# Optimization experiments

Measured on AMD Instinct MI355X. Metric: run time of the kernel, lower is better.

Reference implementation:

```python
import jax, jax.numpy as jnp
import numpy as np

BS, T, N, E = 4, 6, 400, 3000
D = 100        # object_dim == state_dim == out_fts (forced by code)
NS = 30        # num states
NOBJ = 300     # object vocab
NET = 10       # n edge types
NSTEPS = 3     # GatedGraphConv n_steps


def setup_inputs() -> dict:
    key = jax.random.key(0)
    ks = jax.random.split(key, 16)
    def nrm(k, shape, s=0.05):
        return jax.random.normal(k, shape, jnp.float32) * s
    return dict(
        class_names=jax.random.randint(ks[0], (BS, T, N), 0, NOBJ),
        states=jax.random.uniform(ks[1], (BS, T, N, NS), jnp.float32),
        edges=jax.random.randint(ks[2], (BS, T, E, 2), 0, N),
        edge_types=jax.random.randint(ks[3], (BS, T, E), 0, NET),
        visibility=jax.random.uniform(ks[4], (BS, T, N), jnp.float32),
        mask_edges=jnp.ones((BS, T, E), jnp.float32),
        obj_emb=nrm(ks[5], (NOBJ, D)),
        state_W=nrm(ks[6], (D, NS)), state_b=jnp.zeros((D,), jnp.float32),
        c1_W=nrm(ks[7], (D, 2 * D)), c1_b=jnp.zeros((D,), jnp.float32),
        c2_W=nrm(ks[8], (D, D)), c2_b=jnp.zeros((D,), jnp.float32),
        edge_embed=nrm(ks[9], (NET, D * D)),
        g_wih=nrm(ks[10], (3 * D, D)), g_whh=nrm(ks[11], (3 * D, D)),
        g_bih=jnp.zeros((3 * D,), jnp.float32), g_bhh=jnp.zeros((3 * D,), jnp.float32),
        o_wih=nrm(ks[12], (3 * D, D)), o_whh=nrm(ks[13], (3 * D, D)),
    )


def _gru(x, h, wih, whh, bih=None, bhh=None):
    # torch.nn.GRUCell semantics
    gi = x @ wih.T
    gh = h @ whh.T
    if bih is not None:
        gi = gi + bih
        gh = gh + bhh
    ir, iz, inn = jnp.split(gi, 3, axis=-1)
    hr, hz, hn = jnp.split(gh, 3, axis=-1)
    r = jax.nn.sigmoid(ir + hr)
    z = jax.nn.sigmoid(iz + hz)
    n = jnp.tanh(inn + r * hn)
    return (1.0 - z) * n + z * h


def reference(class_names, states, edges, edge_types, visibility, mask_edges,
              obj_emb, state_W, state_b, c1_W, c1_b, c2_W, c2_b,
              edge_embed, g_wih, g_whh, g_bih, g_bhh, o_wih, o_whh):
    bs, t_len, n = class_names.shape
    # initial node representation (ClassNameStateRepresentation)
    emb = obj_emb[class_names]                       # [bs,T,N,D]
    st = states @ state_W.T + state_b                # [bs,T,N,D]
    x = jnp.concatenate([emb, st], -1)
    x = jax.nn.relu(x @ c1_W.T + c1_b) @ c2_W.T + c2_b  # [bs,T,N,D]

    off = (jnp.arange(bs) * n)[:, None]              # flatten batch into node axis
    h = jnp.zeros((bs * n, D), x.dtype)              # outer temporal GRU state
    reprs = []
    for t in range(t_len):
        h = _gru(x[:, t].reshape(bs * n, D), h, o_wih, o_whh)  # bias=False
        feat_flat = h                                 # [bs*N, D]
        src = (edges[:, t, :, 0] + off).reshape(-1)   # [bs*E]
        dst = (edges[:, t, :, 1] + off).reshape(-1)
        # per-edge DxD matrices, masked (as in original)
        W = edge_embed[edge_types[:, t].reshape(-1)].reshape(-1, D, D)
        W = W * mask_edges[:, t].reshape(-1)[:, None, None]
        # NOTE: original never updates feat_flat inside the n_steps loop,
        # so every step reads the same source features; we replicate that.
        feat_out = feat_flat
        for _ in range(NSTEPS):
            msg = jnp.einsum('eij,ej->ei', W, feat_flat[src])           # per-edge matvec
            a = jax.ops.segment_sum(msg, dst, num_segments=bs * n)     # scatter-add
            feat_out = _gru(a, feat_flat, g_wih, g_whh, g_bih, g_bhh)
        reprs.append(feat_out.reshape(bs, n, D) * visibility[:, t, :, None])
    node_reprs = jnp.stack(reprs, 1)                  # [bs,T,N,D]
    num_nodes = visibility.sum(-1) + 1e-9             # [bs,T]
    global_repr = (node_reprs * visibility[..., None]).sum(2) / num_nodes[..., None]
    return node_reprs, global_repr
```

## Files before the change

kernel.cpp:

```cpp
#include <hip/hip_runtime.h>

#define BSZ   4
#define TT    6
#define NNODE 400
#define EED   3000
#define DDIM  100
#define NSDIM 30
#define NETYP 10
#define BN    (BSZ*NNODE)
#define NROW  (BSZ*TT*NNODE)
#define NEDGE (BSZ*TT*EED)
#define KPAD  1024

#define OFF_PRE1 0
#define OFF_QT   30000
#define OFF_BQ   33000
#define OFF_BF   33104
#define OFF_WIT  33408
#define OFF_BI   63408
#define OFF_BH   63744
#define OFF_WFH  64080
#define OFF_WFL  85584
#define OFF_WOH  107088
#define OFF_WOL  128592
#define OFF_BWF  150096
#define OFF_BWPK 450096
#define OFF_WHPK 622128
#define OFF_HALL 643632
#define OFF_START 1603632
#define OFF_SE   1613236
#define OFF_INV  1757248
#define OFF_GI   1757280
#define OFF_UB   4982880

typedef __attribute__((ext_vector_type(8))) short bf16x8;
typedef __attribute__((ext_vector_type(4))) float f32x4;

__device__ __forceinline__ float sigf(float v) { return 1.0f / (1.0f + expf(-v)); }

__device__ __forceinline__ short bfc(float f) {
    union { float f; unsigned u; } v; v.f = f;
    unsigned r = v.u + 0x7fffu + ((v.u >> 16) & 1u);
    return (short)(r >> 16);
}

__device__ __forceinline__ float bf2f(short h) {
    union { unsigned u; float f; } x; x.u = ((unsigned)(unsigned short)h) << 16;
    return x.f;
}

__device__ __forceinline__ unsigned cvtpk(float lo, float hi) {
    unsigned r;
    asm("v_cvt_pk_bf16_f32 %0, %1, %2" : "=v"(r) : "v"(lo), "v"(hi));
    return r;
}

__global__ __launch_bounds__(256) void k_front(
    const float* __restrict__ obj_emb, const float* __restrict__ c1_W,
    const float* __restrict__ c1_b, const float* __restrict__ state_W,
    const float* __restrict__ state_b, const float* __restrict__ c2_W,
    const float* __restrict__ c2_b, const float* __restrict__ o_wih,
    const float* __restrict__ o_whh, const float* __restrict__ g_wih,
    const float* __restrict__ g_bih, const float* __restrict__ g_bhh,
    const float* __restrict__ vis, const int* __restrict__ edges,
    const int* __restrict__ etype, const float* __restrict__ emask,
    float* __restrict__ pre1, float* __restrict__ QT, float* __restrict__ bQ,
    float* __restrict__ bfold, float* __restrict__ WiT,
    float* __restrict__ bI, float* __restrict__ bH,
    ushort* __restrict__ WFH, ushort* __restrict__ WFL,
    ushort* __restrict__ WOH, ushort* __restrict__ WOL,
    float* __restrict__ inv_nv, float* __restrict__ gout,
    int* __restrict__ start, int2* __restrict__ sortedE2) {
    int tid = threadIdx.x;
    if (blockIdx.x < 24) {
        __shared__ int hcnt[400];
        __shared__ int hstart[400];
        int c = blockIdx.x;
        int t = c >> 2, b = c & 3;
        int febase = (b * TT + t) * EED;
        for (int i = tid; i < 400; i += 256) hcnt[i] = 0;
        __syncthreads();
        for (int i = tid; i < EED; i += 256)
            atomicAdd(&hcnt[edges[(febase + i) * 2 + 1]], 1);
        __syncthreads();
        if (tid < 64) {
            int lane = tid, carry = 0;
            for (int ch = 0; ch < 7; ++ch) {
                int idx = ch * 64 + lane;
                int orig = (idx < 400) ? hcnt[idx] : 0;
                int v = orig;
                #pragma unroll
                for (int off = 1; off < 64; off <<= 1) {
                    int u = __shfl_up(v, off, 64);
                    if (lane >= off) v += u;
                }
                if (idx < 400) hstart[idx] = carry + (v - orig);
                carry += __shfl(v, 63, 64);
            }
        }
        __syncthreads();
        for (int i = tid; i < 400; i += 256) {
            start[c * 400 + i] = c * EED + hstart[i];
            hcnt[i] = hstart[i];
        }
        if (c == 23 && tid == 0) start[NROW] = NEDGE;
        __syncthreads();
        for (int i = tid; i < EED; i += 256) {
            int fe = febase + i;
            int2 ed = *(const int2*)(edges + fe * 2);
            int pos = atomicAdd(&hcnt[ed.y], 1);
            int g = etype[fe];
            float m = emask[fe];
            sortedE2[c * EED + pos] = make_int2(ed.x | (g << 16), __float_as_int(m));
        }
        return;
    }
    int i = (blockIdx.x - 24) * 256 + tid;
    if (i < 30000) {
        int cls = i / DDIM, d1 = i % DDIM;
        float acc = 0.f;
        for (int k = 0; k < DDIM; ++k)
            acc += obj_emb[cls * DDIM + k] * c1_W[d1 * 2 * DDIM + k];
        pre1[i] = acc;
    } else if (i < 33000) {
        int j = i - 30000, s = j / DDIM, d1 = j % DDIM;
        float acc = 0.f;
        for (int d = 0; d < DDIM; ++d)
            acc += c1_W[d1 * 2 * DDIM + DDIM + d] * state_W[d * NSDIM + s];
        QT[j] = acc;
    } else if (i < 33100) {
        int d1 = i - 33000;
        float acc = c1_b[d1];
        for (int d = 0; d < DDIM; ++d)
            acc += state_b[d] * c1_W[d1 * 2 * DDIM + DDIM + d];
        bQ[d1] = acc;
    } else if (i < 33400) {
        int o = i - 33100;
        float acc = 0.f;
        for (int d = 0; d < DDIM; ++d)
            acc += o_wih[o * DDIM + d] * c2_b[d];
        bfold[o] = acc;
    } else if (i < 76408) {
        int e = i - 33400;
        int j = e & 7, frag = e >> 3;
        int l = frag & 63, ct = (frag >> 6) % 21, kt = frag / (21 * 64);
        int col = ct * 16 + (l & 15);
        int gate = col / 112, dd = col % 112;
        int k = kt * 32 + ((l >> 4) << 3) + j;
        float v = 0.f;
        if (k < DDIM && dd < DDIM) {
            int o = gate * DDIM + dd;
            for (int d = 0; d < DDIM; ++d)
                v += o_wih[o * DDIM + d] * c2_W[d * DDIM + k];
        }
        short hi = bfc(v);
        WFH[frag * 8 + j] = (ushort)hi;
        WFL[frag * 8 + j] = (ushort)bfc(v - bf2f(hi));
    } else if (i < 119416) {
        int e = i - 76408;
        int j = e & 7, frag = e >> 3;
        int l = frag & 63, ct = (frag >> 6) % 21, kt = frag / (21 * 64);
        int col = ct * 16 + (l & 15);
        int gate = col / 112, dd = col % 112;
        int k = kt * 32 + ((l >> 4) << 3) + j;
        float v = 0.f;
        if (k < DDIM && dd < DDIM)
            v = o_whh[(gate * DDIM + dd) * DDIM + k];
        short hi = bfc(v);
        WOH[frag * 8 + j] = (ushort)hi;
        WOL[frag * 8 + j] = (ushort)bfc(v - bf2f(hi));
    } else if (i < 149416) {
        int j = i - 119416, k = j / 300, o = j % 300;
        WiT[j] = g_wih[o * DDIM + k];
    } else if (i < 149752) {
        int col = i - 149416, gate = col / 112, o = col % 112;
        bI[col] = (o < DDIM) ? g_bih[gate * DDIM + o] : 0.f;
    } else if (i < 150088) {
        int col = i - 149752, gate = col / 112, o = col % 112;
        bH[col] = (o < DDIM) ? g_bhh[gate * DDIM + o] : 0.f;
    } else if (i >= 150144 && i < 151680) {
        int g = (i - 150144) >> 6;
        int lane = i & 63;
        float s = 0.f;
        for (int n = lane; n < NNODE; n += 64)
            s += vis[g * NNODE + n];
        #pragma unroll
        for (int off = 32; off > 0; off >>= 1)
            s += __shfl_down(s, off, 64);
        if (lane == 0) inv_nv[g] = 1.f / (s + 1e-9f);
    } else if (i >= 151680 && i < 154080) {
        gout[i - 151680] = 0.f;
    }
}

__global__ __launch_bounds__(448) void k_mid(
    const float* __restrict__ edge_embed, const float* __restrict__ WiT,
    float* __restrict__ BW,
    const int* __restrict__ cls, const float* __restrict__ states,
    const float* __restrict__ pre1, const float* __restrict__ QT,
    const float* __restrict__ bQ, const float* __restrict__ bfold,
    const bf16x8* __restrict__ WFH, const bf16x8* __restrict__ WFL,
    float* __restrict__ GI) {
    __shared__ float st_lds[16 * NSDIM];
    __shared__ float hid_lds[16 * 112];
    __shared__ int cls_lds[16];
    int tid = threadIdx.x;
    if (blockIdx.x < 670) {
        int i = blockIdx.x * 448 + tid;
        if (i < 1000 * 300) {
            int kk = i / 300, go = i % 300;
            int g = kk / DDIM, k = kk % DDIM;
            const float* es = edge_embed + g * DDIM * DDIM + k;
            float acc = 0.f;
            for (int j = 0; j < DDIM; ++j)
                acc += es[j * DDIM] * WiT[j * 300 + go];
            BW[i] = acc;
        }
        return;
    }
    int r0 = (blockIdx.x - 670) * 16;
    for (int idx = tid; idx < 16 * NSDIM; idx += 448) st_lds[idx] = states[r0 * NSDIM + idx];
    if (tid < 16) cls_lds[tid] = cls[r0 + tid];
    __syncthreads();
    #pragma unroll
    for (int u = 0; u < 4; ++u) {
        int it = tid + u * 448;
        if (it < 1600) {
            int n = it / 100, d = it % 100;
            float acc = bQ[d] + pre1[cls_lds[n] * DDIM + d];
            for (int s = 0; s < NSDIM; ++s)
                acc += QT[s * DDIM + d] * st_lds[n * NSDIM + s];
            hid_lds[n * 112 + d] = fmaxf(acc, 0.f);
        }
    }
    __syncthreads();
    int w = tid >> 6, l = tid & 63, rit = l & 15, kgrp = l >> 4;
    f32x4 acc3[3];
    acc3[0] = acc3[1] = acc3[2] = (f32x4){0.f, 0.f, 0.f, 0.f};
    for (int kt = 0; kt < 4; ++kt) {
        bf16x8 Ahi, Alo;
        #pragma unroll
        for (int j = 0; j < 8; ++j) {
            int k = kt * 32 + kgrp * 8 + j;
            float v = (k < DDIM) ? hid_lds[rit * 112 + k] : 0.f;
            short hi = bfc(v);
            Ahi[j] = hi;
            Alo[j] = bfc(v - bf2f(hi));
        }
        #pragma unroll
        for (int p = 0; p < 3; ++p) {
            int ct = w + p * 7;
            bf16x8 Bhi = WFH[(kt * 21 + ct) * 64 + l];
            bf16x8 Blo = WFL[(kt * 21 + ct) * 64 + l];
            acc3[p] = __builtin_amdgcn_mfma_f32_16x16x32_bf16(Ahi, Bhi, acc3[p], 0, 0, 0);
            acc3[p] = __builtin_amdgcn_mfma_f32_16x16x32_bf16(Alo, Bhi, acc3[p], 0, 0, 0);
            acc3[p] = __builtin_amdgcn_mfma_f32_16x16x32_bf16(Ahi, Blo, acc3[p], 0, 0, 0);
        }
    }
    int dd = w * 16 + rit;
    if (dd < DDIM) {
        int b = r0 / (TT * NNODE), t = (r0 / NNODE) % TT, nn0 = r0 % NNODE;
        int trow0 = t * BN + b * NNODE + nn0;
        #pragma unroll
        for (int p = 0; p < 3; ++p) {
            float bias = bfold[p * DDIM + dd];
            #pragma unroll
            for (int j = 0; j < 4; ++j) {
                int row = kgrp * 4 + j;
                GI[(trow0 + row) * 336 + p * 112 + dd] = acc3[p][j] + bias;
            }
        }
    }
}

__global__ __launch_bounds__(448) void k_mid2(const float* __restrict__ GI,
    const bf16x8* __restrict__ WOH, const bf16x8* __restrict__ WOL,
    float* __restrict__ Hall,
    const float* __restrict__ BW, const float* __restrict__ g_whh,
    bf16x8* __restrict__ BWpk, bf16x8* __restrict__ WHpk) {
    __shared__ float h_lds[16 * 112];
    int tid = threadIdx.x;
    if (blockIdx.x >= 100) {
        int i = (blockIdx.x - 100) * 448 + tid;
        if (i < 43008) {
            int l = i & 63, c = (i >> 6) % 21, kt = i / (21 * 64);
            int col = c * 16 + (l & 15);
            int gate = col / 112, o = col % 112;
            bf16x8 r;
            #pragma unroll
            for (int j = 0; j < 8; ++j) {
                int kk = kt * 32 + ((l >> 4) << 3) + j;
                float v = (kk < 1000 && o < DDIM) ? BW[kk * 300 + gate * DDIM + o] : 0.f;
                r[j] = bfc(v);
            }
            BWpk[i] = r;
        } else if (i < 48384) {
            int id = i - 43008;
            int l = id & 63, c = (id >> 6) % 21, kt2 = id / (21 * 64);
            int col = c * 16 + (l & 15);
            int gate = col / 112, o = col % 112;
            bf16x8 r;
            #pragma unroll
            for (int j = 0; j < 8; ++j) {
                int k = kt2 * 32 + ((l >> 4) << 3) + j;
                float v = (k < DDIM && o < DDIM) ? g_whh[(gate * DDIM + o) * DDIM + k] : 0.f;
                r[j] = bfc(v);
            }
            WHpk[id] = r;
        }
        return;
    }
    int bn0 = blockIdx.x * 16;
    for (int idx = tid; idx < 16 * 112; idx += 448) h_lds[idx] = 0.f;
    __syncthreads();
    int w = tid >> 6, l = tid & 63, rit = l & 15, kgrp = l >> 4;
    int dd = w * 16 + rit;
    for (int t = 0; t < TT; ++t) {
        float gir[4], giz[4], gin[4], hold[4];
        if (dd < DDIM) {
            #pragma unroll
            for (int j = 0; j < 4; ++j) {
                int node = kgrp * 4 + j;
                int trow = t * BN + bn0 + node;
                gir[j] = GI[trow * 336 + dd];
                giz[j] = GI[trow * 336 + 112 + dd];
                gin[j] = GI[trow * 336 + 224 + dd];
                hold[j] = h_lds[node * 112 + dd];
            }
        }
        f32x4 a0 = (f32x4){0.f, 0.f, 0.f, 0.f};
        f32x4 a1 = (f32x4){0.f, 0.f, 0.f, 0.f};
        f32x4 a2 = (f32x4){0.f, 0.f, 0.f, 0.f};
        if (t > 0) {
            for (int kt = 0; kt < 4; ++kt) {
                bf16x8 Ahi, Alo;
                #pragma unroll
                for (int j = 0; j < 8; ++j) {
                    int k = kt * 32 + kgrp * 8 + j;
                    float v = (k < DDIM) ? h_lds[rit * 112 + k] : 0.f;
                    short hi = bfc(v);
                    Ahi[j] = hi;
                    Alo[j] = bfc(v - bf2f(hi));
                }
                {
                    bf16x8 Bhi = WOH[(kt * 21 + w) * 64 + l];
                    bf16x8 Blo = WOL[(kt * 21 + w) * 64 + l];
                    a0 = __builtin_amdgcn_mfma_f32_16x16x32_bf16(Ahi, Bhi, a0, 0, 0, 0);
                    a0 = __builtin_amdgcn_mfma_f32_16x16x32_bf16(Alo, Bhi, a0, 0, 0, 0);
                    a0 = __builtin_amdgcn_mfma_f32_16x16x32_bf16(Ahi, Blo, a0, 0, 0, 0);
                }
                {
                    bf16x8 Bhi = WOH[(kt * 21 + w + 7) * 64 + l];
                    bf16x8 Blo = WOL[(kt * 21 + w + 7) * 64 + l];
                    a1 = __builtin_amdgcn_mfma_f32_16x16x32_bf16(Ahi, Bhi, a1, 0, 0, 0);
                    a1 = __builtin_amdgcn_mfma_f32_16x16x32_bf16(Alo, Bhi, a1, 0, 0, 0);
                    a1 = __builtin_amdgcn_mfma_f32_16x16x32_bf16(Ahi, Blo, a1, 0, 0, 0);
                }
                {
                    bf16x8 Bhi = WOH[(kt * 21 + w + 14) * 64 + l];
                    bf16x8 Blo = WOL[(kt * 21 + w + 14) * 64 + l];
                    a2 = __builtin_amdgcn_mfma_f32_16x16x32_bf16(Ahi, Bhi, a2, 0, 0, 0);
                    a2 = __builtin_amdgcn_mfma_f32_16x16x32_bf16(Alo, Bhi, a2, 0, 0, 0);
                    a2 = __builtin_amdgcn_mfma_f32_16x16x32_bf16(Ahi, Blo, a2, 0, 0, 0);
                }
            }
        }
        __syncthreads();
        if (dd < DDIM) {
            #pragma unroll
            for (int j = 0; j < 4; ++j) {
                int node = kgrp * 4 + j;
                int trow = t * BN + bn0 + node;
                float r = sigf(gir[j] + a0[j]);
                float z = sigf(giz[j] + a1[j]);
                float nn = tanhf(gin[j] + r * a2[j]);
                float hnew = (1.f - z) * nn + z * hold[j];
                h_lds[node * 112 + dd] = hnew;
                Hall[trow * DDIM + dd] = hnew;
            }
        }
        __syncthreads();
    }
}

__global__ __launch_bounds__(256) void k_gather(
    const int* __restrict__ start, const int2* __restrict__ sortedE2,
    const float* __restrict__ Hall, unsigned* __restrict__ Ub2) {
    int gid = blockIdx.x * 256 + threadIdx.x;
    int trd = gid >> 6, l = gid & 63;
    int s0 = start[trd], s1 = start[trd + 1];
    int rowbase = (trd / NNODE) * NNODE;
    float acc[16];
    #pragma unroll
    for (int j = 0; j < 16; ++j) acc[j] = 0.f;
    for (int e0 = s0; e0 < s1; e0 += 4) {
        float2 hA[4], hB[4];
        float me[4];
        int ge[4];
        #pragma unroll
        for (int e = 0; e < 4; ++e) {
            int idx = e0 + e;
            int2 rec = (idx < s1) ? sortedE2[idx] : make_int2(0, 0);
            int src = rec.x & 0xffff;
            int g = rec.x >> 16;
            ge[e] = g;
            me[e] = __int_as_float(rec.y);
            const float* hs = Hall + (size_t)(rowbase + src) * DDIM;
            int k0 = g * 100;
            int J0 = k0 >> 7, J1 = (k0 + 99) >> 7;
            int sA = 128 * J0 + 2 * l, sB = 128 * J1 + 2 * l;
            bool aA = (sA >= k0) && (sA < k0 + 100);
            bool aB = (J1 != J0) && (sB >= k0) && (sB < k0 + 100);
            hA[e] = aA ? *(const float2*)(hs + (sA - k0)) : make_float2(0.f, 0.f);
            hB[e] = aB ? *(const float2*)(hs + (sB - k0)) : make_float2(0.f, 0.f);
        }
        #pragma unroll
        for (int e = 0; e < 4; ++e) {
            float m = me[e];
            float ax = m * hA[e].x, ay = m * hA[e].y;
            float bx = m * hB[e].x, by = m * hB[e].y;
            switch (ge[e]) {
                case 0: acc[0] += ax; acc[1] += ay; break;
                case 1: acc[0] += ax; acc[1] += ay; acc[2] += bx; acc[3] += by; break;
                case 2: acc[2] += ax; acc[3] += ay; acc[4] += bx; acc[5] += by; break;
                case 3: acc[4] += ax; acc[5] += ay; acc[6] += bx; acc[7] += by; break;
                case 4: acc[6] += ax; acc[7] += ay; break;
                case 5: acc[6] += ax; acc[7] += ay; acc[8] += bx; acc[9] += by; break;
                case 6: acc[8] += ax; acc[9] += ay; acc[10] += bx; acc[11] += by; break;
                case 7: acc[10] += ax; acc[11] += ay; acc[12] += bx; acc[13] += by; break;
                case 8: acc[12] += ax; acc[13] += ay; acc[14] += bx; acc[15] += by; break;
                case 9: acc[14] += ax; acc[15] += ay; break;
            }
        }
    }
    unsigned* urow = Ub2 + (size_t)trd * 512;
    #pragma unroll
    for (int j = 0; j < 8; ++j)
        urow[64 * j + l] = cvtpk(acc[2 * j], acc[2 * j + 1]);
}

__global__ __launch_bounds__(448) void k_fused32(const ushort* __restrict__ Ub,
    const bf16x8* __restrict__ BWpk, const bf16x8* __restrict__ WHpk,
    const float* __restrict__ bI, const float* __restrict__ bH,
    const float* __restrict__ Hall, const float* __restrict__ visv,
    const float* __restrict__ inv_nv, float* __restrict__ out,
    float* __restrict__ gout) {
    __shared__ unsigned lds[16384];
    int tid = threadIdx.x;
    int w = tid >> 6, l = tid & 63;
    int rit = l & 15, kgrp = l >> 4;
    int rbase = blockIdx.x * 32;

    for (int i = tid; i < 4096; i += 448) {
        int row = i >> 7, g16 = i & 127;
        int4 wv = *(const int4*)(Ub + (size_t)(rbase + row) * KPAD + g16 * 8);
        int wd = row * 512 + ((g16 * 4) ^ ((row & 7) << 2));
        *(int4*)&lds[wd] = wv;
    }
    __syncthreads();

    f32x4 acc[2][3];
    #pragma unroll
    for (int mt = 0; mt < 2; ++mt)
        #pragma unroll
        for (int q = 0; q < 3; ++q) acc[mt][q] = (f32x4){0.f, 0.f, 0.f, 0.f};

    for (int kt = 0; kt < 32; ++kt) {
        bf16x8 fb0 = BWpk[(kt * 21 + w) * 64 + l];
        bf16x8 fb1 = BWpk[(kt * 21 + w + 7) * 64 + l];
        bf16x8 fb2 = BWpk[(kt * 21 + w + 14) * 64 + l];
        #pragma unroll
        for (int mt = 0; mt < 2; ++mt) {
            int row = mt * 16 + rit;
            int wd = row * 512 + (((kt * 16 + kgrp * 4)) ^ ((row & 7) << 2));
            bf16x8 fa = *(bf16x8*)&lds[wd];
            acc[mt][0] = __builtin_amdgcn_mfma_f32_16x16x32_bf16(fa, fb0, acc[mt][0], 0, 0, 0);
            acc[mt][1] = __builtin_amdgcn_mfma_f32_16x16x32_bf16(fa, fb1, acc[mt][1], 0, 0, 0);
            acc[mt][2] = __builtin_amdgcn_mfma_f32_16x16x32_bf16(fa, fb2, acc[mt][2], 0, 0, 0);
        }
    }
    __syncthreads();

    for (int i = tid; i < 512; i += 448) {
        int row = i >> 4, g16 = i & 15;
        int k0 = g16 * 8;
        const float* hs = Hall + (size_t)(rbase + row) * DDIM;
        float v[8];
        #pragma unroll
        for (int jj = 0; jj < 8; ++jj)
            v[jj] = (k0 + jj < DDIM) ? hs[k0 + jj] : 0.f;
        int4 wv;
        wv.x = (int)cvtpk(v[0], v[1]);
        wv.y = (int)cvtpk(v[2], v[3]);
        wv.z = (int)cvtpk(v[4], v[5]);
        wv.w = (int)cvtpk(v[6], v[7]);
        int wd = row * 64 + ((g16 * 4) ^ ((row & 7) << 2));
        *(int4*)&lds[wd] = wv;
    }
    __syncthreads();

    f32x4 hacc[2];
    hacc[0] = (f32x4){0.f, 0.f, 0.f, 0.f};
    hacc[1] = (f32x4){0.f, 0.f, 0.f, 0.f};
    for (int kt2 = 0; kt2 < 4; ++kt2) {
        bf16x8 fb0 = WHpk[(kt2 * 21 + w) * 64 + l];
        bf16x8 fb1 = WHpk[(kt2 * 21 + w + 7) * 64 + l];
        bf16x8 fb2 = WHpk[(kt2 * 21 + w + 14) * 64 + l];
        #pragma unroll
        for (int mt = 0; mt < 2; ++mt) {
            int row = mt * 16 + rit;
            int wd = row * 64 + (((kt2 * 16 + kgrp * 4)) ^ ((row & 7) << 2));
            bf16x8 fh = *(bf16x8*)&lds[wd];
            acc[mt][0] = __builtin_amdgcn_mfma_f32_16x16x32_bf16(fh, fb0, acc[mt][0], 0, 0, 0);
            acc[mt][1] = __builtin_amdgcn_mfma_f32_16x16x32_bf16(fh, fb1, acc[mt][1], 0, 0, 0);
            hacc[mt]  = __builtin_amdgcn_mfma_f32_16x16x32_bf16(fh, fb2, hacc[mt], 0, 0, 0);
        }
    }

    int col = w * 16 + rit;
    if (col < DDIM) {
        float bIr = bI[col], bIz = bI[112 + col], bIn = bI[224 + col];
        float bHr = bH[col], bHz = bH[112 + col], bHn = bH[224 + col];
        int t = rbase / BN;
        #pragma unroll
        for (int mt = 0; mt < 2; ++mt) {
            int r2 = (rbase + mt * 16) % BN;
            int b = r2 / NNODE, n0 = r2 % NNODE;
            int bt = b * TT + t;
            int trow0 = rbase + mt * 16 + kgrp * 4;
            int brow0 = bt * NNODE + n0 + kgrp * 4;
            float gs = 0.f;
            #pragma unroll
            for (int j = 0; j < 4; ++j) {
                float r = sigf(acc[mt][0][j] + bIr + bHr);
                float z = sigf(acc[mt][1][j] + bIz + bHz);
                float ghn = hacc[mt][j] + bHn;
                float nn = tanhf(acc[mt][2][j] + bIn + r * ghn);
                float hold = Hall[(trow0 + j) * DDIM + col];
                float feat = (1.f - z) * nn + z * hold;
                int brow = brow0 + j;
                float v = visv[brow];
                float outv = feat * v;
                out[brow * DDIM + col] = outv;
                gs += outv * v;
            }
            gs += __shfl_xor(gs, 16, 64);
            gs += __shfl_xor(gs, 32, 64);
            if (kgrp == 0)
                atomicAdd(&gout[bt * DDIM + col], gs * inv_nv[bt]);
        }
    }
}

extern "C" void kernel_launch(void* const* d_in, const int* in_sizes, int n_in,
                              void* d_out, int out_size, void* d_ws, size_t ws_size,
                              hipStream_t stream) {
    const int*   class_names = (const int*)d_in[0];
    const float* states      = (const float*)d_in[1];
    const int*   edges       = (const int*)d_in[2];
    const int*   edge_types  = (const int*)d_in[3];
    const float* visibility  = (const float*)d_in[4];
    const float* mask_edges  = (const float*)d_in[5];
    const float* obj_emb     = (const float*)d_in[6];
    const float* state_W     = (const float*)d_in[7];
    const float* state_b     = (const float*)d_in[8];
    const float* c1_W        = (const float*)d_in[9];
    const float* c1_b        = (const float*)d_in[10];
    const float* c2_W        = (const float*)d_in[11];
    const float* c2_b        = (const float*)d_in[12];
    const float* edge_embed  = (const float*)d_in[13];
    const float* g_wih       = (const float*)d_in[14];
    const float* g_whh       = (const float*)d_in[15];
    const float* g_bih       = (const float*)d_in[16];
    const float* g_bhh       = (const float*)d_in[17];
    const float* o_wih       = (const float*)d_in[18];
    const float* o_whh       = (const float*)d_in[19];

    float* out = (float*)d_out;
    float* gout = out + (size_t)NROW * DDIM;
    float* ws  = (float*)d_ws;
    float*  pre1  = ws + OFF_PRE1;
    float*  QT    = ws + OFF_QT;
    float*  bQ    = ws + OFF_BQ;
    float*  bfold = ws + OFF_BF;
    float*  WiT   = ws + OFF_WIT;
    float*  bI    = ws + OFF_BI;
    float*  bH    = ws + OFF_BH;
    ushort* WFH   = (ushort*)(ws + OFF_WFH);
    ushort* WFL   = (ushort*)(ws + OFF_WFL);
    ushort* WOH   = (ushort*)(ws + OFF_WOH);
    ushort* WOL   = (ushort*)(ws + OFF_WOL);
    float*  BWf   = ws + OFF_BWF;
    bf16x8* BWpk  = (bf16x8*)(ws + OFF_BWPK);
    bf16x8* WHpk  = (bf16x8*)(ws + OFF_WHPK);
    float*  Hall  = ws + OFF_HALL;
    int*    start = (int*)(ws + OFF_START);
    int2*   sortedE2 = (int2*)(ws + OFF_SE);
    float*  inv_nv= ws + OFF_INV;
    float*  GI    = ws + OFF_GI;
    ushort* Ub    = (ushort*)(ws + OFF_UB);

    k_front<<<626, 256, 0, stream>>>(obj_emb, c1_W, c1_b, state_W, state_b,
                                     c2_W, c2_b, o_wih, o_whh, g_wih, g_bih, g_bhh,
                                     visibility, edges, edge_types, mask_edges,
                                     pre1, QT, bQ, bfold, WiT, bI, bH,
                                     WFH, WFL, WOH, WOL, inv_nv, gout,
                                     start, sortedE2);
    k_mid<<<1270, 448, 0, stream>>>(edge_embed, WiT, BWf, class_names, states,
                                    pre1, QT, bQ, bfold,
                                    (const bf16x8*)WFH, (const bf16x8*)WFL, GI);
    k_mid2<<<208, 448, 0, stream>>>(GI, (const bf16x8*)WOH, (const bf16x8*)WOL,
                                    Hall, BWf, g_whh, BWpk, WHpk);
    k_gather<<<NROW / 4, 256, 0, stream>>>(start, sortedE2, Hall, (unsigned*)Ub);
    k_fused32<<<NROW / 32, 448, 0, stream>>>(Ub, BWpk, WHpk, bI, bH, Hall,
                                             visibility, inv_nv, out, gout);
}
```

Measured before the change: 104.6 us.

## Merge five kernels into one persistent kernel with grid-wide barriers

```diff
diff --git a/kernel.cpp b/kernel.cpp
--- a/kernel.cpp
+++ b/kernel.cpp
@@ -10,7 +10,7 @@
 #define BN    (BSZ*NNODE)
 #define NROW  (BSZ*TT*NNODE)
 #define NEDGE (BSZ*TT*EED)
-#define KPAD  1024
+#define NBLK  300
 
 #define OFF_PRE1 0
 #define OFF_QT   30000
@@ -31,7 +31,7 @@
 #define OFF_SE   1613236
 #define OFF_INV  1757248
 #define OFF_GI   1757280
-#define OFF_UB   4982880
+#define OFF_BAR  4982880
 
 typedef __attribute__((ext_vector_type(8))) short bf16x8;
 typedef __attribute__((ext_vector_type(4))) float f32x4;
@@ -55,32 +55,66 @@
     return r;
 }
 
-__global__ __launch_bounds__(256) void k_front(
-    const float* __restrict__ obj_emb, const float* __restrict__ c1_W,
-    const float* __restrict__ c1_b, const float* __restrict__ state_W,
-    const float* __restrict__ state_b, const float* __restrict__ c2_W,
-    const float* __restrict__ c2_b, const float* __restrict__ o_wih,
-    const float* __restrict__ o_whh, const float* __restrict__ g_wih,
+__device__ __forceinline__ void gsync(int* bar) {
+    __syncthreads();
+    if (threadIdx.x == 0) {
+        __threadfence();
+        atomicAdd(bar, 1);
+        while (atomicAdd(bar, 0) < NBLK)
+            __builtin_amdgcn_s_sleep(2);
+        __threadfence();
+    }
+    __syncthreads();
+}
+
+__global__ __launch_bounds__(448, 4) void k_mega(
+    const int* __restrict__ cls, const float* __restrict__ states,
+    const int* __restrict__ edges, const int* __restrict__ etype,
+    const float* __restrict__ emask, const float* __restrict__ vis,
+    const float* __restrict__ obj_emb, const float* __restrict__ state_W,
+    const float* __restrict__ state_b, const float* __restrict__ c1_W,
+    const float* __restrict__ c1_b, const float* __restrict__ c2_W,
+    const float* __restrict__ c2_b, const float* __restrict__ edge_embed,
+    const float* __restrict__ g_wih, const float* __restrict__ g_whh,
     const float* __restrict__ g_bih, const float* __restrict__ g_bhh,
-    const float* __restrict__ vis, const int* __restrict__ edges,
-    const int* __restrict__ etype, const float* __restrict__ emask,
-    float* __restrict__ pre1, float* __restrict__ QT, float* __restrict__ bQ,
-    float* __restrict__ bfold, float* __restrict__ WiT,
-    float* __restrict__ bI, float* __restrict__ bH,
-    ushort* __restrict__ WFH, ushort* __restrict__ WFL,
-    ushort* __restrict__ WOH, ushort* __restrict__ WOL,
-    float* __restrict__ inv_nv, float* __restrict__ gout,
-    int* __restrict__ start, int2* __restrict__ sortedE2) {
+    const float* __restrict__ o_wih, const float* __restrict__ o_whh,
+    float* __restrict__ ws, float* __restrict__ out, float* __restrict__ gout) {
+    __shared__ unsigned lds_u[16384];
     int tid = threadIdx.x;
-    if (blockIdx.x < 24) {
-        __shared__ int hcnt[400];
-        __shared__ int hstart[400];
-        int c = blockIdx.x;
+    int bid = blockIdx.x;
+    int w = tid >> 6, l = tid & 63;
+    int rit = l & 15, kgrp = l >> 4;
+
+    float*  pre1  = ws + OFF_PRE1;
+    float*  QT    = ws + OFF_QT;
+    float*  bQ    = ws + OFF_BQ;
+    float*  bfold = ws + OFF_BF;
+    float*  WiT   = ws + OFF_WIT;
+    float*  bI    = ws + OFF_BI;
+    float*  bH    = ws + OFF_BH;
+    ushort* WFHu  = (ushort*)(ws + OFF_WFH);
+    ushort* WFLu  = (ushort*)(ws + OFF_WFL);
+    ushort* WOHu  = (ushort*)(ws + OFF_WOH);
+    ushort* WOLu  = (ushort*)(ws + OFF_WOL);
+    float*  BW    = ws + OFF_BWF;
+    bf16x8* BWpk  = (bf16x8*)(ws + OFF_BWPK);
+    bf16x8* WHpk  = (bf16x8*)(ws + OFF_WHPK);
+    float*  Hall  = ws + OFF_HALL;
+    int*    start = (int*)(ws + OFF_START);
+    int2*   sortedE2 = (int2*)(ws + OFF_SE);
+    float*  inv_nv = ws + OFF_INV;
+    float*  GI    = ws + OFF_GI;
+    int*    bar   = (int*)(ws + OFF_BAR);
+
+    if (bid < 24) {
+        int* hcnt = (int*)lds_u;
+        int* hstart = hcnt + 400;
+        int c = bid;
         int t = c >> 2, b = c & 3;
         int febase = (b * TT + t) * EED;
-        for (int i = tid; i < 400; i += 256) hcnt[i] = 0;
+        for (int i = tid; i < 400; i += 448) hcnt[i] = 0;
         __syncthreads();
-        for (int i = tid; i < EED; i += 256)
+        for (int i = tid; i < EED; i += 448)
             atomicAdd(&hcnt[edges[(febase + i) * 2 + 1]], 1);
         __syncthreads();
         if (tid < 64) {
@@ -99,13 +133,13 @@
             }
         }
         __syncthreads();
-        for (int i = tid; i < 400; i += 256) {
+        for (int i = tid; i < 400; i += 448) {
             start[c * 400 + i] = c * EED + hstart[i];
             hcnt[i] = hstart[i];
         }
         if (c == 23 && tid == 0) start[NROW] = NEDGE;
         __syncthreads();
-        for (int i = tid; i < EED; i += 256) {
+        for (int i = tid; i < EED; i += 448) {
             int fe = febase + i;
             int2 ed = *(const int2*)(edges + fe * 2);
             int pos = atomicAdd(&hcnt[ed.y], 1);
@@ -113,101 +147,150 @@
             float m = emask[fe];
             sortedE2[c * EED + pos] = make_int2(ed.x | (g << 16), __float_as_int(m));
         }
-        return;
-    }
-    int i = (blockIdx.x - 24) * 256 + tid;
-    if (i < 30000) {
-        int cls = i / DDIM, d1 = i % DDIM;
-        float acc = 0.f;
-        for (int k = 0; k < DDIM; ++k)
-            acc += obj_emb[cls * DDIM + k] * c1_W[d1 * 2 * DDIM + k];
-        pre1[i] = acc;
-    } else if (i < 33000) {
-        int j = i - 30000, s = j / DDIM, d1 = j % DDIM;
-        float acc = 0.f;
-        for (int d = 0; d < DDIM; ++d)
-            acc += c1_W[d1 * 2 * DDIM + DDIM + d] * state_W[d * NSDIM + s];
-        QT[j] = acc;
-    } else if (i < 33100) {
-        int d1 = i - 33000;
-        float acc = c1_b[d1];
-        for (int d = 0; d < DDIM; ++d)
-            acc += state_b[d] * c1_W[d1 * 2 * DDIM + DDIM + d];
-        bQ[d1] = acc;
-    } else if (i < 33400) {
-        int o = i - 33100;
-        float acc = 0.f;
-        for (int d = 0; d < DDIM; ++d)
-            acc += o_wih[o * DDIM + d] * c2_b[d];
-        bfold[o] = acc;
-    } else if (i < 76408) {
-        int e = i - 33400;
-        int j = e & 7, frag = e >> 3;
-        int l = frag & 63, ct = (frag >> 6) % 21, kt = frag / (21 * 64);
-        int col = ct * 16 + (l & 15);
-        int gate = col / 112, dd = col % 112;
-        int k = kt * 32 + ((l >> 4) << 3) + j;
-        float v = 0.f;
-        if (k < DDIM && dd < DDIM) {
-            int o = gate * DDIM + dd;
-            for (int d = 0; d < DDIM; ++d)
-                v += o_wih[o * DDIM + d] * c2_W[d * DDIM + k];
-        }
-        short hi = bfc(v);
-        WFH[frag * 8 + j] = (ushort)hi;
-        WFL[frag * 8 + j] = (ushort)bfc(v - bf2f(hi));
-    } else if (i < 119416) {
-        int e = i - 76408;
-        int j = e & 7, frag = e >> 3;
-        int l = frag & 63, ct = (frag >> 6) % 21, kt = frag / (21 * 64);
-        int col = ct * 16 + (l & 15);
-        int gate = col / 112, dd = col % 112;
-        int k = kt * 32 + ((l >> 4) << 3) + j;
-        float v = 0.f;
-        if (k < DDIM && dd < DDIM)
-            v = o_whh[(gate * DDIM + dd) * DDIM + k];
-        short hi = bfc(v);
-        WOH[frag * 8 + j] = (ushort)hi;
-        WOL[frag * 8 + j] = (ushort)bfc(v - bf2f(hi));
-    } else if (i < 149416) {
-        int j = i - 119416, k = j / 300, o = j % 300;
-        WiT[j] = g_wih[o * DDIM + k];
-    } else if (i < 149752) {
-        int col = i - 149416, gate = col / 112, o = col % 112;
-        bI[col] = (o < DDIM) ? g_bih[gate * DDIM + o] : 0.f;
-    } else if (i < 150088) {
-        int col = i - 149752, gate = col / 112, o = col % 112;
-        bH[col] = (o < DDIM) ? g_bhh[gate * DDIM + o] : 0.f;
-    } else if (i >= 150144 && i < 151680) {
-        int g = (i - 150144) >> 6;
-        int lane = i & 63;
-        float s = 0.f;
-        for (int n = lane; n < NNODE; n += 64)
-            s += vis[g * NNODE + n];
-        #pragma unroll
-        for (int off = 32; off > 0; off >>= 1)
-            s += __shfl_down(s, off, 64);
-        if (lane == 0) inv_nv[g] = 1.f / (s + 1e-9f);
-    } else if (i >= 151680 && i < 154080) {
-        gout[i - 151680] = 0.f;
-    }
-}
-
-__global__ __launch_bounds__(448) void k_mid(
-    const float* __restrict__ edge_embed, const float* __restrict__ WiT,
-    float* __restrict__ BW,
-    const int* __restrict__ cls, const float* __restrict__ states,
-    const float* __restrict__ pre1, const float* __restrict__ QT,
-    const float* __restrict__ bQ, const float* __restrict__ bfold,
-    const bf16x8* __restrict__ WFH, const bf16x8* __restrict__ WFL,
-    float* __restrict__ GI) {
-    __shared__ float st_lds[16 * NSDIM];
-    __shared__ float hid_lds[16 * 112];
-    __shared__ int cls_lds[16];
-    int tid = threadIdx.x;
-    if (blockIdx.x < 670) {
-        int i = blockIdx.x * 448 + tid;
-        if (i < 1000 * 300) {
+    } else {
+        for (int i = (bid - 24) * 448 + tid; i < 154080; i += 276 * 448) {
+            if (i < 30000) {
+                int cc = i / DDIM, d1 = i % DDIM;
+                float acc = 0.f;
+                for (int k = 0; k < DDIM; ++k)
+                    acc += obj_emb[cc * DDIM + k] * c1_W[d1 * 2 * DDIM + k];
+                pre1[i] = acc;
+            } else if (i < 33000) {
+                int j = i - 30000, s = j / DDIM, d1 = j % DDIM;
+                float acc = 0.f;
+                for (int d = 0; d < DDIM; ++d)
+                    acc += c1_W[d1 * 2 * DDIM + DDIM + d] * state_W[d * NSDIM + s];
+                QT[j] = acc;
+            } else if (i < 33100) {
+                int d1 = i - 33000;
+                float acc = c1_b[d1];
+                for (int d = 0; d < DDIM; ++d)
+                    acc += state_b[d] * c1_W[d1 * 2 * DDIM + DDIM + d];
+                bQ[d1] = acc;
+            } else if (i < 33400) {
+                int o = i - 33100;
+                float acc = 0.f;
+                for (int d = 0; d < DDIM; ++d)
+                    acc += o_wih[o * DDIM + d] * c2_b[d];
+                bfold[o] = acc;
+            } else if (i < 76408) {
+                int e = i - 33400;
+                int j = e & 7, frag = e >> 3;
+                int ll = frag & 63, ct = (frag >> 6) % 21, kt = frag / (21 * 64);
+                int col = ct * 16 + (ll & 15);
+                int gate = col / 112, dd = col % 112;
+                int k = kt * 32 + ((ll >> 4) << 3) + j;
+                float v = 0.f;
+                if (k < DDIM && dd < DDIM) {
+                    int o = gate * DDIM + dd;
+                    for (int d = 0; d < DDIM; ++d)
+                        v += o_wih[o * DDIM + d] * c2_W[d * DDIM + k];
+                }
+                short hi = bfc(v);
+                WFHu[frag * 8 + j] = (ushort)hi;
+                WFLu[frag * 8 + j] = (ushort)bfc(v - bf2f(hi));
+            } else if (i < 119416) {
+                int e = i - 76408;
+                int j = e & 7, frag = e >> 3;
+                int ll = frag & 63, ct = (frag >> 6) % 21, kt = frag / (21 * 64);
+                int col = ct * 16 + (ll & 15);
+                int gate = col / 112, dd = col % 112;
+                int k = kt * 32 + ((ll >> 4) << 3) + j;
+                float v = 0.f;
+                if (k < DDIM && dd < DDIM)
+                    v = o_whh[(gate * DDIM + dd) * DDIM + k];
+                short hi = bfc(v);
+                WOHu[frag * 8 + j] = (ushort)hi;
+                WOLu[frag * 8 + j] = (ushort)bfc(v - bf2f(hi));
+            } else if (i < 149416) {
+                int j = i - 119416, k = j / 300, o = j % 300;
+                WiT[j] = g_wih[o * DDIM + k];
+            } else if (i < 149752) {
+                int col = i - 149416, gate = col / 112, o = col % 112;
+                bI[col] = (o < DDIM) ? g_bih[gate * DDIM + o] : 0.f;
+            } else if (i < 150088) {
+                int col = i - 149752, gate = col / 112, o = col % 112;
+                bH[col] = (o < DDIM) ? g_bhh[gate * DDIM + o] : 0.f;
+            } else if (i >= 150144 && i < 151680) {
+                int g = (i - 150144) >> 6;
+                int lane = i & 63;
+                float s = 0.f;
+                for (int n = lane; n < NNODE; n += 64)
+                    s += vis[g * NNODE + n];
+                #pragma unroll
+                for (int off = 32; off > 0; off >>= 1)
+                    s += __shfl_down(s, off, 64);
+                if (lane == 0) inv_nv[g] = 1.f / (s + 1e-9f);
+            } else if (i >= 151680 && i < 154080) {
+                gout[i - 151680] = 0.f;
+            }
+        }
+    }
+    gsync(&bar[0]);
+
+    {
+        float* st_lds = (float*)lds_u;
+        float* hid_lds = st_lds + 480;
+        int* cls_lds = (int*)(hid_lds + 1792);
+        const bf16x8* WFH = (const bf16x8*)WFHu;
+        const bf16x8* WFL = (const bf16x8*)WFLu;
+        for (int tile = bid; tile < 600; tile += 300) {
+            int r0 = tile * 16;
+            for (int idx = tid; idx < 16 * NSDIM; idx += 448)
+                st_lds[idx] = states[r0 * NSDIM + idx];
+            if (tid < 16) cls_lds[tid] = cls[r0 + tid];
+            __syncthreads();
+            #pragma unroll
+            for (int u = 0; u < 4; ++u) {
+                int it = tid + u * 448;
+                if (it < 1600) {
+                    int n = it / 100, d = it % 100;
+                    float acc = bQ[d] + pre1[cls_lds[n] * DDIM + d];
+                    for (int s = 0; s < NSDIM; ++s)
+                        acc += QT[s * DDIM + d] * st_lds[n * NSDIM + s];
+                    hid_lds[n * 112 + d] = fmaxf(acc, 0.f);
+                }
+            }
+            __syncthreads();
+            f32x4 acc3[3];
+            acc3[0] = acc3[1] = acc3[2] = (f32x4){0.f, 0.f, 0.f, 0.f};
+            for (int kt = 0; kt < 4; ++kt) {
+                bf16x8 Ahi, Alo;
+                #pragma unroll
+                for (int j = 0; j < 8; ++j) {
+                    int k = kt * 32 + kgrp * 8 + j;
+                    float v = (k < DDIM) ? hid_lds[rit * 112 + k] : 0.f;
+                    short hi = bfc(v);
+                    Ahi[j] = hi;
+                    Alo[j] = bfc(v - bf2f(hi));
+                }
+                #pragma unroll
+                for (int p = 0; p < 3; ++p) {
+                    int ct = w + p * 7;
+                    bf16x8 Bhi = WFH[(kt * 21 + ct) * 64 + l];
+                    bf16x8 Blo = WFL[(kt * 21 + ct) * 64 + l];
+                    acc3[p] = __builtin_amdgcn_mfma_f32_16x16x32_bf16(Ahi, Bhi, acc3[p], 0, 0, 0);
+                    acc3[p] = __builtin_amdgcn_mfma_f32_16x16x32_bf16(Alo, Bhi, acc3[p], 0, 0, 0);
+                    acc3[p] = __builtin_amdgcn_mfma_f32_16x16x32_bf16(Ahi, Blo, acc3[p], 0, 0, 0);
+                }
+            }
+            int dd = w * 16 + rit;
+            if (dd < DDIM) {
+                int b = r0 / (TT * NNODE), t = (r0 / NNODE) % TT, nn0 = r0 % NNODE;
+                int trow0 = t * BN + b * NNODE + nn0;
+                #pragma unroll
+                for (int p = 0; p < 3; ++p) {
+                    float bias = bfold[p * DDIM + dd];
+                    #pragma unroll
+                    for (int j = 0; j < 4; ++j) {
+                        int row = kgrp * 4 + j;
+                        GI[(trow0 + row) * 336 + p * 112 + dd] = acc3[p][j] + bias;
+                    }
+                }
+            }
+            __syncthreads();
+        }
+        for (int i = bid * 448 + tid; i < 300000; i += 300 * 448) {
             int kk = i / 300, go = i % 300;
             int g = kk / DDIM, k = kk % DDIM;
             const float* es = edge_embed + g * DDIM * DDIM + k;
@@ -216,267 +299,194 @@
                 acc += es[j * DDIM] * WiT[j * 300 + go];
             BW[i] = acc;
         }
-        return;
-    }
-    int r0 = (blockIdx.x - 670) * 16;
-    for (int idx = tid; idx < 16 * NSDIM; idx += 448) st_lds[idx] = states[r0 * NSDIM + idx];
-    if (tid < 16) cls_lds[tid] = cls[r0 + tid];
-    __syncthreads();
-    #pragma unroll
-    for (int u = 0; u < 4; ++u) {
-        int it = tid + u * 448;
-        if (it < 1600) {
-            int n = it / 100, d = it % 100;
-            float acc = bQ[d] + pre1[cls_lds[n] * DDIM + d];
-            for (int s = 0; s < NSDIM; ++s)
-                acc += QT[s * DDIM + d] * st_lds[n * NSDIM + s];
-            hid_lds[n * 112 + d] = fmaxf(acc, 0.f);
-        }
-    }
-    __syncthreads();
-    int w = tid >> 6, l = tid & 63, rit = l & 15, kgrp = l >> 4;
-    f32x4 acc3[3];
-    acc3[0] = acc3[1] = acc3[2] = (f32x4){0.f, 0.f, 0.f, 0.f};
-    for (int kt = 0; kt < 4; ++kt) {
-        bf16x8 Ahi, Alo;
-        #pragma unroll
-        for (int j = 0; j < 8; ++j) {
-            int k = kt * 32 + kgrp * 8 + j;
-            float v = (k < DDIM) ? hid_lds[rit * 112 + k] : 0.f;
-            short hi = bfc(v);
-            Ahi[j] = hi;
-            Alo[j] = bfc(v - bf2f(hi));
-        }
-        #pragma unroll
-        for (int p = 0; p < 3; ++p) {
-            int ct = w + p * 7;
-            bf16x8 Bhi = WFH[(kt * 21 + ct) * 64 + l];
-            bf16x8 Blo = WFL[(kt * 21 + ct) * 64 + l];
-            acc3[p] = __builtin_amdgcn_mfma_f32_16x16x32_bf16(Ahi, Bhi, acc3[p], 0, 0, 0);
-            acc3[p] = __builtin_amdgcn_mfma_f32_16x16x32_bf16(Alo, Bhi, acc3[p], 0, 0, 0);
-            acc3[p] = __builtin_amdgcn_mfma_f32_16x16x32_bf16(Ahi, Blo, acc3[p], 0, 0, 0);
-        }
-    }
-    int dd = w * 16 + rit;
-    if (dd < DDIM) {
-        int b = r0 / (TT * NNODE), t = (r0 / NNODE) % TT, nn0 = r0 % NNODE;
-        int trow0 = t * BN + b * NNODE + nn0;
-        #pragma unroll
-        for (int p = 0; p < 3; ++p) {
-            float bias = bfold[p * DDIM + dd];
-            #pragma unroll
-            for (int j = 0; j < 4; ++j) {
-                int row = kgrp * 4 + j;
-                GI[(trow0 + row) * 336 + p * 112 + dd] = acc3[p][j] + bias;
-            }
-        }
-    }
-}
-
-__global__ __launch_bounds__(448) void k_mid2(const float* __restrict__ GI,
-    const bf16x8* __restrict__ WOH, const bf16x8* __restrict__ WOL,
-    float* __restrict__ Hall,
-    const float* __restrict__ BW, const float* __restrict__ g_whh,
-    bf16x8* __restrict__ BWpk, bf16x8* __restrict__ WHpk) {
-    __shared__ float h_lds[16 * 112];
-    int tid = threadIdx.x;
-    if (blockIdx.x >= 100) {
-        int i = (blockIdx.x - 100) * 448 + tid;
+    }
+    gsync(&bar[1]);
+
+    if (bid < 100) {
+        float* h_lds = (float*)lds_u;
+        const bf16x8* WOH = (const bf16x8*)WOHu;
+        const bf16x8* WOL = (const bf16x8*)WOLu;
+        int bn0 = bid * 16;
+        for (int idx = tid; idx < 16 * 112; idx += 448) h_lds[idx] = 0.f;
+        __syncthreads();
+        int dd = w * 16 + rit;
+        for (int t = 0; t < TT; ++t) {
+            float gir[4], giz[4], gin[4], hold[4];
+            if (dd < DDIM) {
+                #pragma unroll
+                for (int j = 0; j < 4; ++j) {
+                    int node = kgrp * 4 + j;
+                    int trow = t * BN + bn0 + node;
+                    gir[j] = GI[trow * 336 + dd];
+                    giz[j] = GI[trow * 336 + 112 + dd];
+                    gin[j] = GI[trow * 336 + 224 + dd];
+                    hold[j] = h_lds[node * 112 + dd];
+                }
+            }
+            f32x4 a0 = (f32x4){0.f, 0.f, 0.f, 0.f};
+            f32x4 a1 = (f32x4){0.f, 0.f, 0.f, 0.f};
+            f32x4 a2 = (f32x4){0.f, 0.f, 0.f, 0.f};
+            if (t > 0) {
+                for (int kt = 0; kt < 4; ++kt) {
+                    bf16x8 Ahi, Alo;
+                    #pragma unroll
+                    for (int j = 0; j < 8; ++j) {
+                        int k = kt * 32 + kgrp * 8 + j;
+                        float v = (k < DDIM) ? h_lds[rit * 112 + k] : 0.f;
+                        short hi = bfc(v);
+                        Ahi[j] = hi;
+                        Alo[j] = bfc(v - bf2f(hi));
+                    }
+                    {
+                        bf16x8 Bhi = WOH[(kt * 21 + w) * 64 + l];
+                        bf16x8 Blo = WOL[(kt * 21 + w) * 64 + l];
+                        a0 = __builtin_amdgcn_mfma_f32_16x16x32_bf16(Ahi, Bhi, a0, 0, 0, 0);
+                        a0 = __builtin_amdgcn_mfma_f32_16x16x32_bf16(Alo, Bhi, a0, 0, 0, 0);
+                        a0 = __builtin_amdgcn_mfma_f32_16x16x32_bf16(Ahi, Blo, a0, 0, 0, 0);
+                    }
+                    {
+                        bf16x8 Bhi = WOH[(kt * 21 + w + 7) * 64 + l];
+                        bf16x8 Blo = WOL[(kt * 21 + w + 7) * 64 + l];
+                        a1 = __builtin_amdgcn_mfma_f32_16x16x32_bf16(Ahi, Bhi, a1, 0, 0, 0);
+                        a1 = __builtin_amdgcn_mfma_f32_16x16x32_bf16(Alo, Bhi, a1, 0, 0, 0);
+                        a1 = __builtin_amdgcn_mfma_f32_16x16x32_bf16(Ahi, Blo, a1, 0, 0, 0);
+                    }
+                    {
+                        bf16x8 Bhi = WOH[(kt * 21 + w + 14) * 64 + l];
+                        bf16x8 Blo = WOL[(kt * 21 + w + 14) * 64 + l];
+                        a2 = __builtin_amdgcn_mfma_f32_16x16x32_bf16(Ahi, Bhi, a2, 0, 0, 0);
+                        a2 = __builtin_amdgcn_mfma_f32_16x16x32_bf16(Alo, Bhi, a2, 0, 0, 0);
+                        a2 = __builtin_amdgcn_mfma_f32_16x16x32_bf16(Ahi, Blo, a2, 0, 0, 0);
+                    }
+                }
+            }
+            __syncthreads();
+            if (dd < DDIM) {
+                #pragma unroll
+                for (int j = 0; j < 4; ++j) {
+                    int node = kgrp * 4 + j;
+                    int trow = t * BN + bn0 + node;
+                    float r = sigf(gir[j] + a0[j]);
+                    float z = sigf(giz[j] + a1[j]);
+                    float nn = tanhf(gin[j] + r * a2[j]);
+                    float hnew = (1.f - z) * nn + z * hold[j];
+                    h_lds[node * 112 + dd] = hnew;
+                    Hall[trow * DDIM + dd] = hnew;
+                }
+            }
+            __syncthreads();
+        }
+    } else if (bid < 208) {
+        int i = (bid - 100) * 448 + tid;
         if (i < 43008) {
-            int l = i & 63, c = (i >> 6) % 21, kt = i / (21 * 64);
-            int col = c * 16 + (l & 15);
+            int ll = i & 63, c = (i >> 6) % 21, kt = i / (21 * 64);
+            int col = c * 16 + (ll & 15);
             int gate = col / 112, o = col % 112;
             bf16x8 r;
             #pragma unroll
             for (int j = 0; j < 8; ++j) {
-                int kk = kt * 32 + ((l >> 4) << 3) + j;
+                int kk = kt * 32 + ((ll >> 4) << 3) + j;
                 float v = (kk < 1000 && o < DDIM) ? BW[kk * 300 + gate * DDIM + o] : 0.f;
                 r[j] = bfc(v);
             }
             BWpk[i] = r;
         } else if (i < 48384) {
             int id = i - 43008;
-            int l = id & 63, c = (id >> 6) % 21, kt2 = id / (21 * 64);
-            int col = c * 16 + (l & 15);
+            int ll = id & 63, c = (id >> 6) % 21, kt2 = id / (21 * 64);
+            int col = c * 16 + (ll & 15);
             int gate = col / 112, o = col % 112;
             bf16x8 r;
             #pragma unroll
             for (int j = 0; j < 8; ++j) {
-                int k = kt2 * 32 + ((l >> 4) << 3) + j;
+                int k = kt2 * 32 + ((ll >> 4) << 3) + j;
                 float v = (k < DDIM && o < DDIM) ? g_whh[(gate * DDIM + o) * DDIM + k] : 0.f;
                 r[j] = bfc(v);
             }
             WHpk[id] = r;
         }
-        return;
-    }
-    int bn0 = blockIdx.x * 16;
-    for (int idx = tid; idx < 16 * 112; idx += 448) h_lds[idx] = 0.f;
+    }
+    gsync(&bar[2]);
+
+    int rbase = bid * 32;
+    for (int r = w; r < 32; r += 7) {
+        int trd = rbase + r;
+        int s0 = start[trd], s1 = start[trd + 1];
+        int rowbase = (trd / NNODE) * NNODE;
+        float acc[16];
+        #pragma unroll
+        for (int j = 0; j < 16; ++j) acc[j] = 0.f;
+        for (int e0 = s0; e0 < s1; e0 += 4) {
+            float2 hA[4], hB[4];
+            float me[4];
+            int ge[4];
+            #pragma unroll
+            for (int e = 0; e < 4; ++e) {
+                int idx = e0 + e;
+                int2 rec = (idx < s1) ? sortedE2[idx] : make_int2(0, 0);
+                int src = rec.x & 0xffff;
+                int g = rec.x >> 16;
+                ge[e] = g;
+                me[e] = __int_as_float(rec.y);
+                const float* hs = Hall + (size_t)(rowbase + src) * DDIM;
+                int k0 = g * 100;
+                int J0 = k0 >> 7, J1 = (k0 + 99) >> 7;
+                int sA = 128 * J0 + 2 * l, sB = 128 * J1 + 2 * l;
+                bool aA = (sA >= k0) && (sA < k0 + 100);
+                bool aB = (J1 != J0) && (sB >= k0) && (sB < k0 + 100);
+                hA[e] = aA ? *(const float2*)(hs + (sA - k0)) : make_float2(0.f, 0.f);
+                hB[e] = aB ? *(const float2*)(hs + (sB - k0)) : make_float2(0.f, 0.f);
+            }
+            #pragma unroll
+            for (int e = 0; e < 4; ++e) {
+                float m = me[e];
+                float ax = m * hA[e].x, ay = m * hA[e].y;
+                float bx = m * hB[e].x, by = m * hB[e].y;
+                switch (ge[e]) {
+                    case 0: acc[0] += ax; acc[1] += ay; break;
+                    case 1: acc[0] += ax; acc[1] += ay; acc[2] += bx; acc[3] += by; break;
+                    case 2: acc[2] += ax; acc[3] += ay; acc[4] += bx; acc[5] += by; break;
+                    case 3: acc[4] += ax; acc[5] += ay; acc[6] += bx; acc[7] += by; break;
+                    case 4: acc[6] += ax; acc[7] += ay; break;
+                    case 5: acc[6] += ax; acc[7] += ay; acc[8] += bx; acc[9] += by; break;
+                    case 6: acc[8] += ax; acc[9] += ay; acc[10] += bx; acc[11] += by; break;
+                    case 7: acc[10] += ax; acc[11] += ay; acc[12] += bx; acc[13] += by; break;
+                    case 8: acc[12] += ax; acc[13] += ay; acc[14] += bx; acc[15] += by; break;
+                    case 9: acc[14] += ax; acc[15] += ay; break;
+                }
+            }
+        }
+        #pragma unroll
+        for (int j = 0; j < 8; ++j) {
+            unsigned word = cvtpk(acc[2 * j], acc[2 * j + 1]);
+            int g16 = 16 * j + (l >> 2);
+            int wd = r * 512 + ((g16 * 4) ^ ((r & 7) << 2)) + (l & 3);
+            lds_u[wd] = word;
+        }
+    }
     __syncthreads();
-    int w = tid >> 6, l = tid & 63, rit = l & 15, kgrp = l >> 4;
-    int dd = w * 16 + rit;
-    for (int t = 0; t < TT; ++t) {
-        float gir[4], giz[4], gin[4], hold[4];
-        if (dd < DDIM) {
-            #pragma unroll
-            for (int j = 0; j < 4; ++j) {
-                int node = kgrp * 4 + j;
-                int trow = t * BN + bn0 + node;
-                gir[j] = GI[trow * 336 + dd];
-                giz[j] = GI[trow * 336 + 112 + dd];
-                gin[j] = GI[trow * 336 + 224 + dd];
-                hold[j] = h_lds[node * 112 + dd];
-            }
-        }
-        f32x4 a0 = (f32x4){0.f, 0.f, 0.f, 0.f};
-        f32x4 a1 = (f32x4){0.f, 0.f, 0.f, 0.f};
-        f32x4 a2 = (f32x4){0.f, 0.f, 0.f, 0.f};
-        if (t > 0) {
-            for (int kt = 0; kt < 4; ++kt) {
-                bf16x8 Ahi, Alo;
-                #pragma unroll
-                for (int j = 0; j < 8; ++j) {
-                    int k = kt * 32 + kgrp * 8 + j;
-                    float v = (k < DDIM) ? h_lds[rit * 112 + k] : 0.f;
-                    short hi = bfc(v);
-                    Ahi[j] = hi;
-                    Alo[j] = bfc(v - bf2f(hi));
-                }
-                {
-                    bf16x8 Bhi = WOH[(kt * 21 + w) * 64 + l];
-                    bf16x8 Blo = WOL[(kt * 21 + w) * 64 + l];
-                    a0 = __builtin_amdgcn_mfma_f32_16x16x32_bf16(Ahi, Bhi, a0, 0, 0, 0);
-                    a0 = __builtin_amdgcn_mfma_f32_16x16x32_bf16(Alo, Bhi, a0, 0, 0, 0);
-                    a0 = __builtin_amdgcn_mfma_f32_16x16x32_bf16(Ahi, Blo, a0, 0, 0, 0);
-                }
-                {
-                    bf16x8 Bhi = WOH[(kt * 21 + w + 7) * 64 + l];
-                    bf16x8 Blo = WOL[(kt * 21 + w + 7) * 64 + l];
-                    a1 = __builtin_amdgcn_mfma_f32_16x16x32_bf16(Ahi, Bhi, a1, 0, 0, 0);
-                    a1 = __builtin_amdgcn_mfma_f32_16x16x32_bf16(Alo, Bhi, a1, 0, 0, 0);
-                    a1 = __builtin_amdgcn_mfma_f32_16x16x32_bf16(Ahi, Blo, a1, 0, 0, 0);
-                }
-                {
-                    bf16x8 Bhi = WOH[(kt * 21 + w + 14) * 64 + l];
-                    bf16x8 Blo = WOL[(kt * 21 + w + 14) * 64 + l];
-                    a2 = __builtin_amdgcn_mfma_f32_16x16x32_bf16(Ahi, Bhi, a2, 0, 0, 0);
-                    a2 = __builtin_amdgcn_mfma_f32_16x16x32_bf16(Alo, Bhi, a2, 0, 0, 0);
-                    a2 = __builtin_amdgcn_mfma_f32_16x16x32_bf16(Ahi, Blo, a2, 0, 0, 0);
-                }
-            }
-        }
-        __syncthreads();
-        if (dd < DDIM) {
-            #pragma unroll
-            for (int j = 0; j < 4; ++j) {
-                int node = kgrp * 4 + j;
-                int trow = t * BN + bn0 + node;
-                float r = sigf(gir[j] + a0[j]);
-                float z = sigf(giz[j] + a1[j]);
-                float nn = tanhf(gin[j] + r * a2[j]);
-                float hnew = (1.f - z) * nn + z * hold[j];
-                h_lds[node * 112 + dd] = hnew;
-                Hall[trow * DDIM + dd] = hnew;
-            }
-        }
-        __syncthreads();
-    }
-}
-
-__global__ __launch_bounds__(256) void k_gather(
-    const int* __restrict__ start, const int2* __restrict__ sortedE2,
-    const float* __restrict__ Hall, unsigned* __restrict__ Ub2) {
-    int gid = blockIdx.x * 256 + threadIdx.x;
-    int trd = gid >> 6, l = gid & 63;
-    int s0 = start[trd], s1 = start[trd + 1];
-    int rowbase = (trd / NNODE) * NNODE;
-    float acc[16];
-    #pragma unroll
-    for (int j = 0; j < 16; ++j) acc[j] = 0.f;
-    for (int e0 = s0; e0 < s1; e0 += 4) {
-        float2 hA[4], hB[4];
-        float me[4];
-        int ge[4];
-        #pragma unroll
-        for (int e = 0; e < 4; ++e) {
-            int idx = e0 + e;
-            int2 rec = (idx < s1) ? sortedE2[idx] : make_int2(0, 0);
-            int src = rec.x & 0xffff;
-            int g = rec.x >> 16;
-            ge[e] = g;
-            me[e] = __int_as_float(rec.y);
-            const float* hs = Hall + (size_t)(rowbase + src) * DDIM;
-            int k0 = g * 100;
-            int J0 = k0 >> 7, J1 = (k0 + 99) >> 7;
-            int sA = 128 * J0 + 2 * l, sB = 128 * J1 + 2 * l;
-            bool aA = (sA >= k0) && (sA < k0 + 100);
-            bool aB = (J1 != J0) && (sB >= k0) && (sB < k0 + 100);
-            hA[e] = aA ? *(const float2*)(hs + (sA - k0)) : make_float2(0.f, 0.f);
-            hB[e] = aB ? *(const float2*)(hs + (sB - k0)) : make_float2(0.f, 0.f);
-        }
-        #pragma unroll
-        for (int e = 0; e < 4; ++e) {
-            float m = me[e];
-            float ax = m * hA[e].x, ay = m * hA[e].y;
-            float bx = m * hB[e].x, by = m * hB[e].y;
-            switch (ge[e]) {
-                case 0: acc[0] += ax; acc[1] += ay; break;
-                case 1: acc[0] += ax; acc[1] += ay; acc[2] += bx; acc[3] += by; break;
-                case 2: acc[2] += ax; acc[3] += ay; acc[4] += bx; acc[5] += by; break;
-                case 3: acc[4] += ax; acc[5] += ay; acc[6] += bx; acc[7] += by; break;
-                case 4: acc[6] += ax; acc[7] += ay; break;
-                case 5: acc[6] += ax; acc[7] += ay; acc[8] += bx; acc[9] += by; break;
-                case 6: acc[8] += ax; acc[9] += ay; acc[10] += bx; acc[11] += by; break;
-                case 7: acc[10] += ax; acc[11] += ay; acc[12] += bx; acc[13] += by; break;
-                case 8: acc[12] += ax; acc[13] += ay; acc[14] += bx; acc[15] += by; break;
-                case 9: acc[14] += ax; acc[15] += ay; break;
-            }
-        }
-    }
-    unsigned* urow = Ub2 + (size_t)trd * 512;
-    #pragma unroll
-    for (int j = 0; j < 8; ++j)
-        urow[64 * j + l] = cvtpk(acc[2 * j], acc[2 * j + 1]);
-}
-
-__global__ __launch_bounds__(448) void k_fused32(const ushort* __restrict__ Ub,
-    const bf16x8* __restrict__ BWpk, const bf16x8* __restrict__ WHpk,
-    const float* __restrict__ bI, const float* __restrict__ bH,
-    const float* __restrict__ Hall, const float* __restrict__ visv,
-    const float* __restrict__ inv_nv, float* __restrict__ out,
-    float* __restrict__ gout) {
-    __shared__ unsigned lds[16384];
-    int tid = threadIdx.x;
-    int w = tid >> 6, l = tid & 63;
-    int rit = l & 15, kgrp = l >> 4;
-    int rbase = blockIdx.x * 32;
-
-    for (int i = tid; i < 4096; i += 448) {
-        int row = i >> 7, g16 = i & 127;
-        int4 wv = *(const int4*)(Ub + (size_t)(rbase + row) * KPAD + g16 * 8);
-        int wd = row * 512 + ((g16 * 4) ^ ((row & 7) << 2));
-        *(int4*)&lds[wd] = wv;
-    }
-    __syncthreads();
-
-    f32x4 acc[2][3];
+
+    f32x4 acc4[2][3];
     #pragma unroll
     for (int mt = 0; mt < 2; ++mt)
         #pragma unroll
-        for (int q = 0; q < 3; ++q) acc[mt][q] = (f32x4){0.f, 0.f, 0.f, 0.f};
-
+        for (int q = 0; q < 3; ++q) acc4[mt][q] = (f32x4){0.f, 0.f, 0.f, 0.f};
+
+    bf16x8 nb0 = BWpk[(0 * 21 + w) * 64 + l];
+    bf16x8 nb1 = BWpk[(0 * 21 + w + 7) * 64 + l];
+    bf16x8 nb2 = BWpk[(0 * 21 + w + 14) * 64 + l];
     for (int kt = 0; kt < 32; ++kt) {
-        bf16x8 fb0 = BWpk[(kt * 21 + w) * 64 + l];
-        bf16x8 fb1 = BWpk[(kt * 21 + w + 7) * 64 + l];
-        bf16x8 fb2 = BWpk[(kt * 21 + w + 14) * 64 + l];
+        bf16x8 fb0 = nb0, fb1 = nb1, fb2 = nb2;
+        nb0 = BWpk[((kt + 1) * 21 + w) * 64 + l];
+        nb1 = BWpk[((kt + 1) * 21 + w + 7) * 64 + l];
+        nb2 = BWpk[((kt + 1) * 21 + w + 14) * 64 + l];
         #pragma unroll
         for (int mt = 0; mt < 2; ++mt) {
             int row = mt * 16 + rit;
             int wd = row * 512 + (((kt * 16 + kgrp * 4)) ^ ((row & 7) << 2));
-            bf16x8 fa = *(bf16x8*)&lds[wd];
-            acc[mt][0] = __builtin_amdgcn_mfma_f32_16x16x32_bf16(fa, fb0, acc[mt][0], 0, 0, 0);
-            acc[mt][1] = __builtin_amdgcn_mfma_f32_16x16x32_bf16(fa, fb1, acc[mt][1], 0, 0, 0);
-            acc[mt][2] = __builtin_amdgcn_mfma_f32_16x16x32_bf16(fa, fb2, acc[mt][2], 0, 0, 0);
+            bf16x8 fa = *(bf16x8*)&lds_u[wd];
+            acc4[mt][0] = __builtin_amdgcn_mfma_f32_16x16x32_bf16(fa, fb0, acc4[mt][0], 0, 0, 0);
+            acc4[mt][1] = __builtin_amdgcn_mfma_f32_16x16x32_bf16(fa, fb1, acc4[mt][1], 0, 0, 0);
+            acc4[mt][2] = __builtin_amdgcn_mfma_f32_16x16x32_bf16(fa, fb2, acc4[mt][2], 0, 0, 0);
         }
     }
     __syncthreads();
@@ -495,7 +505,7 @@
         wv.z = (int)cvtpk(v[4], v[5]);
         wv.w = (int)cvtpk(v[6], v[7]);
         int wd = row * 64 + ((g16 * 4) ^ ((row & 7) << 2));
-        *(int4*)&lds[wd] = wv;
+        *(int4*)&lds_u[wd] = wv;
     }
     __syncthreads();
 
@@ -510,9 +520,9 @@
         for (int mt = 0; mt < 2; ++mt) {
             int row = mt * 16 + rit;
             int wd = row * 64 + (((kt2 * 16 + kgrp * 4)) ^ ((row & 7) << 2));
-            bf16x8 fh = *(bf16x8*)&lds[wd];
-            acc[mt][0] = __builtin_amdgcn_mfma_f32_16x16x32_bf16(fh, fb0, acc[mt][0], 0, 0, 0);
-            acc[mt][1] = __builtin_amdgcn_mfma_f32_16x16x32_bf16(fh, fb1, acc[mt][1], 0, 0, 0);
+            bf16x8 fh = *(bf16x8*)&lds_u[wd];
+            acc4[mt][0] = __builtin_amdgcn_mfma_f32_16x16x32_bf16(fh, fb0, acc4[mt][0], 0, 0, 0);
+            acc4[mt][1] = __builtin_amdgcn_mfma_f32_16x16x32_bf16(fh, fb1, acc4[mt][1], 0, 0, 0);
             hacc[mt]  = __builtin_amdgcn_mfma_f32_16x16x32_bf16(fh, fb2, hacc[mt], 0, 0, 0);
         }
     }
@@ -532,14 +542,14 @@
             float gs = 0.f;
             #pragma unroll
             for (int j = 0; j < 4; ++j) {
-                float r = sigf(acc[mt][0][j] + bIr + bHr);
-                float z = sigf(acc[mt][1][j] + bIz + bHz);
+                float r = sigf(acc4[mt][0][j] + bIr + bHr);
+                float z = sigf(acc4[mt][1][j] + bIz + bHz);
                 float ghn = hacc[mt][j] + bHn;
-                float nn = tanhf(acc[mt][2][j] + bIn + r * ghn);
+                float nn = tanhf(acc4[mt][2][j] + bIn + r * ghn);
                 float hold = Hall[(trow0 + j) * DDIM + col];
                 float feat = (1.f - z) * nn + z * hold;
                 int brow = brow0 + j;
-                float v = visv[brow];
+                float v = vis[brow];
                 float outv = feat * v;
                 out[brow * DDIM + col] = outv;
                 gs += outv * v;
@@ -579,39 +589,12 @@
     float* out = (float*)d_out;
     float* gout = out + (size_t)NROW * DDIM;
     float* ws  = (float*)d_ws;
-    float*  pre1  = ws + OFF_PRE1;
-    float*  QT    = ws + OFF_QT;
-    float*  bQ    = ws + OFF_BQ;
-    float*  bfold = ws + OFF_BF;
-    float*  WiT   = ws + OFF_WIT;
-    float*  bI    = ws + OFF_BI;
-    float*  bH    = ws + OFF_BH;
-    ushort* WFH   = (ushort*)(ws + OFF_WFH);
-    ushort* WFL   = (ushort*)(ws + OFF_WFL);
-    ushort* WOH   = (ushort*)(ws + OFF_WOH);
-    ushort* WOL   = (ushort*)(ws + OFF_WOL);
-    float*  BWf   = ws + OFF_BWF;
-    bf16x8* BWpk  = (bf16x8*)(ws + OFF_BWPK);
-    bf16x8* WHpk  = (bf16x8*)(ws + OFF_WHPK);
-    float*  Hall  = ws + OFF_HALL;
-    int*    start = (int*)(ws + OFF_START);
-    int2*   sortedE2 = (int2*)(ws + OFF_SE);
-    float*  inv_nv= ws + OFF_INV;
-    float*  GI    = ws + OFF_GI;
-    ushort* Ub    = (ushort*)(ws + OFF_UB);
-
-    k_front<<<626, 256, 0, stream>>>(obj_emb, c1_W, c1_b, state_W, state_b,
-                                     c2_W, c2_b, o_wih, o_whh, g_wih, g_bih, g_bhh,
-                                     visibility, edges, edge_types, mask_edges,
-                                     pre1, QT, bQ, bfold, WiT, bI, bH,
-                                     WFH, WFL, WOH, WOL, inv_nv, gout,
-                                     start, sortedE2);
-    k_mid<<<1270, 448, 0, stream>>>(edge_embed, WiT, BWf, class_names, states,
-                                    pre1, QT, bQ, bfold,
-                                    (const bf16x8*)WFH, (const bf16x8*)WFL, GI);
-    k_mid2<<<208, 448, 0, stream>>>(GI, (const bf16x8*)WOH, (const bf16x8*)WOL,
-                                    Hall, BWf, g_whh, BWpk, WHpk);
-    k_gather<<<NROW / 4, 256, 0, stream>>>(start, sortedE2, Hall, (unsigned*)Ub);
-    k_fused32<<<NROW / 32, 448, 0, stream>>>(Ub, BWpk, WHpk, bI, bH, Hall,
-                                             visibility, inv_nv, out, gout);
+
+    hipMemsetAsync(ws + OFF_BAR, 0, 4 * sizeof(int), stream);
+
+    k_mega<<<NBLK, 448, 0, stream>>>(class_names, states, edges, edge_types,
+                                     mask_edges, visibility, obj_emb, state_W,
+                                     state_b, c1_W, c1_b, c2_W, c2_b, edge_embed,
+                                     g_wih, g_whh, g_bih, g_bhh, o_wih, o_whh,
+                                     ws, out, gout);
 }
```

Result: slower. 299.0 us (+185.7%).
